# Performance work log

Measured on AMD Instinct MI355X. Metric: run time of the kernel, lower is better.

The kernel has to match this reference:

```python
import jax, jax.numpy as jnp
import numpy as np

HEADS = 20  # SDXL-style: hidden_size 1280 / head_dim 64
IP_SCALE = 1.0


def setup_inputs() -> dict:
    key = jax.random.key(0)
    ks = jax.random.split(key, 12)
    B, Sq, T, C, D, NIP = 4, 4096, 77, 1280, 2048, 16
    s = lambda fan: 1.0 / np.sqrt(fan)
    # post-softmax multiplicative mask: col 0 (sot token) forced to 1, rest a binary spatial mask
    spat = (jax.random.uniform(ks[0], (1, Sq, 1)) < 0.5).astype(jnp.float32)
    attention_mask = jnp.concatenate([jnp.ones((1, Sq, 1)), jnp.tile(spat, (1, 1, T - 1))], axis=-1)
    return {
        "hidden_states": jax.random.normal(ks[1], (B, Sq, C), jnp.float32),
        "encoder_hidden_states": jax.random.normal(ks[2], (B, T, D), jnp.float32),
        "ip_hidden_states": jax.random.normal(ks[3], (B, NIP, D), jnp.float32),
        "attention_mask": attention_mask,
        "Wq": jax.random.normal(ks[4], (C, C), jnp.float32) * s(C),
        "Wk": jax.random.normal(ks[5], (D, C), jnp.float32) * s(D),
        "Wv": jax.random.normal(ks[6], (D, C), jnp.float32) * s(D),
        "Wo": jax.random.normal(ks[7], (C, C), jnp.float32) * s(C),
        "bo": jnp.zeros((C,), jnp.float32),
        "Wk_ip": jax.random.normal(ks[8], (D, C), jnp.float32) * s(D),
        "Wv_ip": jax.random.normal(ks[9], (D, C), jnp.float32) * s(D),
    }


def reference(hidden_states, encoder_hidden_states, ip_hidden_states, attention_mask,
              Wq, Wk, Wv, Wo, bo, Wk_ip, Wv_ip):
    B, Sq, C = hidden_states.shape
    H = HEADS
    d = C // H
    scale = d ** -0.5
    # projections (torch Linear with weights stored [in, out])
    q = (hidden_states @ Wq).reshape(B, Sq, H, d)
    k = (encoder_hidden_states @ Wk).reshape(B, -1, H, d)
    v = (encoder_hidden_states @ Wv).reshape(B, -1, H, d)
    # explicit QK^T softmax, then POST-softmax multiplicative mask (as in get_attention_scores + mask multiply)
    scores = jnp.einsum('bqhd,bkhd->bhqk', q, k) * scale
    probs = jax.nn.softmax(scores, axis=-1)
    probs = probs * attention_mask[:, None, :, :]  # [1,1,Sq,T] broadcast over batch*heads
    out = jnp.einsum('bhqk,bkhd->bqhd', probs, v).reshape(B, Sq, C)
    out = out @ Wo + bo  # to_out[0]; to_out[1] is dropout (identity at eval)
    # IP-adapter stream (single stream, no spatial ip mask): standard SDPA against ip tokens
    k_ip = (ip_hidden_states @ Wk_ip).reshape(B, -1, H, d)
    v_ip = (ip_hidden_states @ Wv_ip).reshape(B, -1, H, d)
    s_ip = jnp.einsum('bqhd,bkhd->bhqk', q, k_ip) * scale
    p_ip = jax.nn.softmax(s_ip, axis=-1)
    ip_out = jnp.einsum('bhqk,bkhd->bqhd', p_ip, v_ip).reshape(B, Sq, C)
    return out + IP_SCALE * ip_out
```

## Files before the change

### kernel.cpp

```cpp
#include <hip/hip_runtime.h>

typedef __attribute__((ext_vector_type(4))) float f32x4;
typedef __attribute__((ext_vector_type(8))) short s16x8;
typedef __attribute__((ext_vector_type(8))) __bf16 bf16x8;
typedef unsigned short u16;

__device__ __forceinline__ u16 f2b(float f) {
  union { float f; unsigned u; } x; x.f = f;
  unsigned r = x.u + 0x7fffu + ((x.u >> 16) & 1u);
  return (u16)(r >> 16);
}
__device__ __forceinline__ float b2f(u16 u) {
  union { unsigned u; float f; } x; x.u = ((unsigned)u) << 16;
  return x.f;
}
__device__ __forceinline__ void gld16(const void* g, void* l) {
  __builtin_amdgcn_global_load_lds(
      (const __attribute__((address_space(1))) unsigned int*)g,
      (__attribute__((address_space(3))) unsigned int*)l, 16, 0, 0);
}
__device__ __forceinline__ f32x4 mfma_bf16(s16x8 a, s16x8 b, f32x4 c) {
  return __builtin_amdgcn_mfma_f32_16x16x32_bf16(
      __builtin_bit_cast(bf16x8, a), __builtin_bit_cast(bf16x8, b), c, 0, 0, 0);
}

#define BAR() asm volatile("s_barrier" ::: "memory")

__global__ void k_convert_all(const float* __restrict__ hs, const float* __restrict__ ehs,
                              const float* __restrict__ iph,
                              u16* __restrict__ hsb, u16* __restrict__ ehsb,
                              u16* __restrict__ ipb) {
  const int n1 = 16384 * 1280 / 4, n2 = 308 * 2048 / 4, n3 = 64 * 2048 / 4;
  int i = blockIdx.x * blockDim.x + threadIdx.x;
  const float* src; u16* dst; int j = i;
  if (i < n1) { src = hs; dst = hsb; }
  else if (i < n1 + n2) { src = ehs; dst = ehsb; j = i - n1; }
  else if (i < n1 + n2 + n3) { src = iph; dst = ipb; j = i - n1 - n2; }
  else return;
  float4 v = ((const float4*)src)[j];
  ushort4 o;
  o.x = f2b(v.x); o.y = f2b(v.y); o.z = f2b(v.z); o.w = f2b(v.w);
  ((ushort4*)dst)[j] = o;
}

__global__ void k_transpose_all(const float* Wk, const float* Wv, const float* Wkip,
                                const float* Wvip, const float* Wq, const float* Wo,
                                u16* TK, u16* TV, u16* TKip, u16* TVip,
                                u16* TQ, u16* TO) {
  const int z = blockIdx.z;
  const float* W = (z == 0) ? Wk : (z == 1) ? Wv : (z == 2) ? Wkip
                  : (z == 3) ? Wvip : (z == 4) ? Wq : Wo;
  u16* T = (z == 0) ? TK : (z == 1) ? TV : (z == 2) ? TKip
          : (z == 3) ? TVip : (z == 4) ? TQ : TO;
  const int K = (z < 4) ? 2048 : 1280;
  const int N = 1280;
  __shared__ float tile[32][33];
  int n0 = blockIdx.x * 32, k0 = blockIdx.y * 32;
  if (k0 >= K) return;
  int tx = threadIdx.x & 31, ty = threadIdx.x >> 5;
#pragma unroll
  for (int i = 0; i < 32; i += 8)
    tile[ty + i][tx] = W[(size_t)(k0 + ty + i) * N + n0 + tx];
  __syncthreads();
#pragma unroll
  for (int i = 0; i < 32; i += 8)
    T[(size_t)(n0 + ty + i) * K + k0 + tx] = f2b(tile[tx][ty + i]);
}

__device__ __forceinline__ void gemm_core0(
    const u16* __restrict__ A, const u16* __restrict__ BT,
    int M, int N, int K, u16* __restrict__ outb, int m0, int n0) {
  const int tid = threadIdx.x;
  const int l = tid & 63;
  const int w = tid >> 6;
  const int wr = w >> 1, wc = w & 1;
  __shared__ u16 As[3][128 * 32];
  __shared__ u16 Bs[3][128 * 32];
  f32x4 acc[4][4] = {};

  const int o0 = tid * 16;
  const int o1 = o0 + 4096;
  const int ra0 = o0 >> 6, ca0 = (o0 & 63) >> 1;
  const int ra1 = o1 >> 6, ca1 = (o1 & 63) >> 1;
  int ga0 = m0 + ra0; if (ga0 >= M) ga0 = M - 1;
  int ga1 = m0 + ra1; if (ga1 >= M) ga1 = M - 1;
  const u16* Ar0 = A + (size_t)ga0 * K + ca0;
  const u16* Ar1 = A + (size_t)ga1 * K + ca1;
  const u16* Br0 = BT + (size_t)(n0 + ra0) * K + ca0;
  const u16* Br1 = BT + (size_t)(n0 + ra1) * K + ca1;

  const int KT = K >> 5;
#define SSTAGE(s, kt)                                 \
  {                                                   \
    const int k0_ = (kt) << 5;                        \
    gld16(Ar0 + k0_, &As[s][o0 >> 1]);                \
    gld16(Ar1 + k0_, &As[s][o1 >> 1]);                \
    gld16(Br0 + k0_, &Bs[s][o0 >> 1]);                \
    gld16(Br1 + k0_, &Bs[s][o1 >> 1]);                \
  }
  SSTAGE(0, 0);
  SSTAGE(1, 1);
  asm volatile("s_waitcnt vmcnt(4)" ::: "memory");
  BAR();

  int slot = 0;
  for (int j = 0; j < KT; ++j) {
    const bool pf = (j + 2 < KT);
    if (pf) {
      int s2 = slot + 2; if (s2 >= 3) s2 -= 3;
      SSTAGE(s2, j + 2);
    }
    s16x8 af[4], bfr[4];
#pragma unroll
    for (int mi = 0; mi < 4; ++mi)
      af[mi] = *(const s16x8*)&As[slot][(wr * 64 + mi * 16 + (l & 15)) * 32 + (l >> 4) * 8];
#pragma unroll
    for (int ni = 0; ni < 4; ++ni)
      bfr[ni] = *(const s16x8*)&Bs[slot][(wc * 64 + ni * 16 + (l & 15)) * 32 + (l >> 4) * 8];
#pragma unroll
    for (int mi = 0; mi < 4; ++mi)
#pragma unroll
      for (int ni = 0; ni < 4; ++ni)
        acc[mi][ni] = mfma_bf16(af[mi], bfr[ni], acc[mi][ni]);
    if (pf) asm volatile("s_waitcnt vmcnt(4)" ::: "memory");
    else    asm volatile("s_waitcnt vmcnt(0)" ::: "memory");
    BAR();
    ++slot; if (slot >= 3) slot = 0;
  }

#pragma unroll
  for (int mi = 0; mi < 4; ++mi) {
    const int mbase = m0 + wr * 64 + mi * 16 + (l >> 4) * 4;
#pragma unroll
    for (int ni = 0; ni < 4; ++ni) {
      const int ncol = n0 + wc * 64 + ni * 16 + (l & 15);
#pragma unroll
      for (int r = 0; r < 4; ++r) {
        int m = mbase + r;
        if (m < M) outb[(size_t)m * N + ncol] = f2b(acc[mi][ni][r]);
      }
    }
  }
#undef SSTAGE
}

__global__ __launch_bounds__(256) void k_gemm_small4(
    const u16* __restrict__ ehsb, const u16* __restrict__ ipb,
    const u16* __restrict__ WkT, const u16* __restrict__ WvT,
    const u16* __restrict__ WkipT, const u16* __restrict__ WvipT,
    u16* kbuf, u16* vbuf, u16* kipb, u16* vipb) {
  const int z = blockIdx.z;
  const int M = (z < 2) ? 308 : 64;
  const int m0 = blockIdx.y * 128;
  if (m0 >= M) return;
  const u16* A = (z < 2) ? ehsb : ipb;
  const u16* BT = (z == 0) ? WkT : (z == 1) ? WvT : (z == 2) ? WkipT : WvipT;
  u16* out = (z == 0) ? kbuf : (z == 1) ? vbuf : (z == 2) ? kipb : vipb;
  gemm_core0(A, BT, M, 1280, 2048, out, m0, blockIdx.x * 128);
}

template <int EPI>
__global__ __launch_bounds__(512, 1) void k_gemm256(
    const u16* __restrict__ A, const u16* __restrict__ BT,
    int N, int K, float alpha,
    u16* __restrict__ outb, float* __restrict__ outf,
    const float* __restrict__ bias, const u16* __restrict__ ipadd,
    int nbx) {
  __shared__ u16 lds[73728];
  const int tid = threadIdx.x, l = tid & 63, w = tid >> 6;
  const int lr = l & 15, lg = l >> 4;
  const int wr = w >> 2, wc = w & 3;
  const bool wlo = (w < 4);

  const int nwg = gridDim.x;
  const int q = nwg >> 3, r = nwg & 7;
  const int xcd = blockIdx.x & 7, lid = blockIdx.x >> 3;
  const int wg = (xcd < r) ? (xcd * (q + 1) + lid)
                           : (r * (q + 1) + (xcd - r) * q + lid);
  const int bm0 = (wg / nbx) * 256, bn0 = (wg % nbx) * 320;

  const int srow = tid >> 2;
  const int sslot = ((tid & 3) ^ ((srow >> 1) & 3)) * 8;
  const size_t aO0 = (size_t)(bm0 + srow) * K + sslot;
  const size_t aO1 = aO0 + (size_t)128 * K;
  const size_t bO0 = (size_t)(bn0 + srow) * K + sslot;
  const size_t bO1 = bO0 + (size_t)128 * K;
  const size_t bO2 = bO0 + (size_t)256 * K;
  const int d0 = tid * 8, d1 = (tid + 512) * 8, d2 = (tid + 1024) * 8;

  const int KT = K >> 5;
  f32x4 acc[8][5] = {};
  s16x8 bfv[5], afv[4];

  const int xsw = (lg ^ ((lr >> 1) & 3)) * 8;
  const int aRow = (wr * 128 + lr) * 32 + xsw;
  const int bRow = 32768 + (wc * 80 + lr) * 32 + xsw;

#define STAGE_A(slot, kt)                                              \
  {                                                                    \
    const int base_ = (slot) * 8192;                                   \
    const size_t go_ = (size_t)(kt) * 32;                              \
    gld16(A + aO0 + go_, &lds[base_ + d0]);                            \
    gld16(A + aO1 + go_, &lds[base_ + d1]);                            \
  }
#define STAGE_B(slot, kt)                                              \
  {                                                                    \
    const int base_ = 32768 + (slot) * 10240;                          \
    const size_t go_ = (size_t)(kt) * 32;                              \
    gld16(BT + bO0 + go_, &lds[base_ + d0]);                           \
    gld16(BT + bO1 + go_, &lds[base_ + d1]);                           \
    if (wlo) gld16(BT + bO2 + go_, &lds[base_ + d2]);                  \
  }
#define WAIT_DEEP()                                                    \
  {                                                                    \
    if (wlo) asm volatile("s_waitcnt vmcnt(10)" ::: "memory");         \
    else     asm volatile("s_waitcnt vmcnt(8)" ::: "memory");          \
  }
#define WAIT_MID()                                                     \
  {                                                                    \
    if (wlo) asm volatile("s_waitcnt vmcnt(5)" ::: "memory");          \
    else     asm volatile("s_waitcnt vmcnt(4)" ::: "memory");          \
  }
#define WAITVM0() asm volatile("s_waitcnt vmcnt(0)" ::: "memory")

  STAGE_A(0, 0); STAGE_B(0, 0);
  STAGE_A(1, 1); STAGE_B(1, 1);
  STAGE_A(2, 2); STAGE_B(2, 2);
  WAIT_DEEP();
  BAR();

  for (int j = 0; j < KT; ++j) {
    const int slot = j & 3;
    const int ab = slot * 8192;
    const int bb = slot * 10240;
    const bool pf = (j + 3 < KT);
    const int s3 = (j + 3) & 3;
#pragma unroll
    for (int ni = 0; ni < 5; ++ni)
      bfv[ni] = *(const s16x8*)&lds[bb + bRow + ni * 512];
#pragma unroll
    for (int mi = 0; mi < 4; ++mi)
      afv[mi] = *(const s16x8*)&lds[ab + aRow + mi * 512];
    if (pf) STAGE_A(s3, j + 3);
    __builtin_amdgcn_s_setprio(1);
#pragma unroll
    for (int mi = 0; mi < 4; ++mi)
#pragma unroll
      for (int ni = 0; ni < 5; ++ni)
        acc[mi][ni] = mfma_bf16(afv[mi], bfv[ni], acc[mi][ni]);
    __builtin_amdgcn_s_setprio(0);
#pragma unroll
    for (int mi = 0; mi < 4; ++mi)
      afv[mi] = *(const s16x8*)&lds[ab + aRow + (mi + 4) * 512];
    if (pf) STAGE_B(s3, j + 3);
    __builtin_amdgcn_s_setprio(1);
#pragma unroll
    for (int mi = 0; mi < 4; ++mi)
#pragma unroll
      for (int ni = 0; ni < 5; ++ni)
        acc[mi + 4][ni] = mfma_bf16(afv[mi], bfv[ni], acc[mi + 4][ni]);
    __builtin_amdgcn_s_setprio(0);
    if (pf) { WAIT_DEEP(); }
    else if (j == KT - 3) { WAIT_MID(); }
    else { WAITVM0(); }
    BAR();
  }

  WAITVM0();
  __syncthreads();

  if constexpr (EPI == 0) {
#pragma unroll
    for (int half = 0; half < 2; ++half) {
      if (half) __syncthreads();
      if (wr == half) {
#pragma unroll
        for (int mi = 0; mi < 8; ++mi) {
          const int row = mi * 16 + lg * 4;
#pragma unroll
          for (int ni = 0; ni < 5; ++ni) {
            const int col = wc * 80 + ni * 16 + lr;
#pragma unroll
            for (int rr = 0; rr < 4; ++rr)
              lds[(row + rr) * 320 + col] = f2b(acc[mi][ni][rr] * alpha);
          }
        }
      }
      __syncthreads();
      const int rbase = tid >> 3;
      const int cseg = tid & 7;
#pragma unroll
      for (int rr2 = 0; rr2 < 2; ++rr2)
#pragma unroll
        for (int jj = 0; jj < 5; ++jj) {
          const int row = rr2 * 64 + rbase;
          const int ch = cseg + jj * 8;
          *(int4*)(outb + (size_t)(bm0 + half * 128 + row) * N + bn0 + ch * 8) =
              *(const int4*)&lds[row * 320 + ch * 8];
        }
    }
  } else {
#pragma unroll
    for (int mi = 0; mi < 8; ++mi) {
      const int mrow = bm0 + wr * 128 + mi * 16 + lg * 4;
#pragma unroll
      for (int ni = 0; ni < 5; ++ni) {
        const int ncol = bn0 + wc * 80 + ni * 16 + lr;
#pragma unroll
        for (int rr = 0; rr < 4; ++rr) {
          const size_t idx = (size_t)(mrow + rr) * N + ncol;
          outf[idx] = acc[mi][ni][rr] + bias[ncol] + b2f(ipadd[idx]);
        }
      }
    }
  }
#undef STAGE_A
#undef STAGE_B
#undef WAIT_DEEP
#undef WAIT_MID
#undef WAITVM0
}

__global__ __launch_bounds__(512, 4) void k_attn(
    const u16* __restrict__ Q,
    const u16* __restrict__ Kb,
    const u16* __restrict__ Vb,
    const u16* __restrict__ Kip,
    const u16* __restrict__ Vip,
    const float* __restrict__ mask,
    u16* __restrict__ Oattn,
    u16* __restrict__ Oip) {
  const int qt = blockIdx.x, h = blockIdx.y, b = blockIdx.z;
  const int tid = threadIdx.x, l = tid & 63, w = tid >> 6;
  const int lr = l & 15, lg = l >> 4;
  const int r0 = w * 16;
  const int m0 = b * 4096 + qt * 128;

  __shared__ u16 KV[192][72];
  __shared__ u16 Ps[128][104];
  __shared__ u16 P2s[128][40];

  const u16* qrow = Q + (size_t)(m0 + r0 + lr) * 1280 + h * 64;
  s16x8 aq0 = *(const s16x8*)(qrow + lg * 8);
  s16x8 aq1 = *(const s16x8*)(qrow + 32 + lg * 8);

  for (int s = tid; s < 192 * 8; s += 512) {
    const int row = s >> 3, seg = s & 7;
    int4 v = {0, 0, 0, 0};
    const u16* src = nullptr;
    if (row < 77)       src = Kb  + (size_t)(b * 77 + row) * 1280 + h * 64 + seg * 8;
    else if (row < 80)  src = nullptr;
    else if (row < 96)  src = Kip + (size_t)(b * 16 + row - 80) * 1280 + h * 64 + seg * 8;
    else if (row < 173) src = Vb  + (size_t)(b * 77 + row - 96) * 1280 + h * 64 + seg * 8;
    else if (row < 176) src = nullptr;
    else                src = Vip + (size_t)(b * 16 + row - 176) * 1280 + h * 64 + seg * 8;
    if (src) v = *(const int4*)src;
    *(int4*)&KV[row][(seg ^ ((row >> 3) & 3)) * 8] = v;
  }
  __syncthreads();

  f32x4 sc[5];
  f32x4 sip = {};
#pragma unroll
  for (int t5 = 0; t5 < 6; ++t5) {
    const int trow = t5 * 16 + lr;
    const int qz = (trow >> 3) & 3;
    s16x8 b0 = *(const s16x8*)&KV[trow][(lg ^ qz) * 8];
    s16x8 b1 = *(const s16x8*)&KV[trow][((lg + 4) ^ qz) * 8];
    f32x4 c = {};
    c = mfma_bf16(aq0, b0, c);
    c = mfma_bf16(aq1, b1, c);
    if (t5 < 5) sc[t5] = c; else sip = c;
  }

#pragma unroll
  for (int r = 0; r < 4; ++r) {
    float mx = fmaxf(fmaxf(fmaxf(sc[0][r], sc[1][r]), fmaxf(sc[2][r], sc[3][r])), sc[4][r]);
    mx = fmaxf(mx, __shfl_xor(mx, 1));
    mx = fmaxf(mx, __shfl_xor(mx, 2));
    mx = fmaxf(mx, __shfl_xor(mx, 4));
    mx = fmaxf(mx, __shfl_xor(mx, 8));
    float p[5], sm = 0.f;
#pragma unroll
    for (int t5 = 0; t5 < 5; ++t5) {
      bool valid = (t5 < 4) | (lr < 13);
      p[t5] = valid ? __expf(sc[t5][r] - mx) : 0.f;
      sm += p[t5];
    }
    sm += __shfl_xor(sm, 1);
    sm += __shfl_xor(sm, 2);
    sm += __shfl_xor(sm, 4);
    sm += __shfl_xor(sm, 8);
    const float inv = 1.0f / sm;
    const int row = r0 + lg * 4 + r;
    const int qg = qt * 128 + row;
#pragma unroll
    for (int t5 = 0; t5 < 5; ++t5) {
      int t = t5 * 16 + lr;
      float pf = 0.f;
      if (t < 77) pf = p[t5] * inv * mask[qg * 77 + t];
      Ps[row][t] = f2b(pf);
    }
    Ps[row][80 + lr] = 0;

    float m2 = sip[r];
    m2 = fmaxf(m2, __shfl_xor(m2, 1));
    m2 = fmaxf(m2, __shfl_xor(m2, 2));
    m2 = fmaxf(m2, __shfl_xor(m2, 4));
    m2 = fmaxf(m2, __shfl_xor(m2, 8));
    float pi = __expf(sip[r] - m2);
    float s2 = pi;
    s2 += __shfl_xor(s2, 1);
    s2 += __shfl_xor(s2, 2);
    s2 += __shfl_xor(s2, 4);
    s2 += __shfl_xor(s2, 8);
    P2s[row][lr] = 0;
    P2s[row][16 + lr] = f2b(pi / s2);
  }

  s16x8 ap[3];
#pragma unroll
  for (int ks = 0; ks < 3; ++ks)
    ap[ks] = *(const s16x8*)&Ps[r0 + lr][ks * 32 + lg * 8];
  s16x8 aip = *(const s16x8*)&P2s[r0 + lr][lg * 8];

  f32x4 om[4], oi[4];
#pragma unroll
  for (int nt = 0; nt < 4; ++nt) {
    const int dcol = (nt * 16 + lr) ^ (lg << 3);
    f32x4 o = {};
#pragma unroll
    for (int ks = 0; ks < 3; ++ks) {
      s16x8 bv;
#pragma unroll
      for (int j = 0; j < 8; ++j)
        bv[j] = (short)KV[96 + ks * 32 + lg * 8 + j][dcol];
      o = mfma_bf16(ap[ks], bv, o);
    }
    s16x8 bip;
#pragma unroll
    for (int j = 0; j < 8; ++j)
      bip[j] = (short)KV[160 + lg * 8 + j][dcol];
    f32x4 o2 = {};
    o2 = mfma_bf16(aip, bip, o2);
    om[nt] = o;
    oi[nt] = o2;
  }

  __syncthreads();

  u16 (*Om)[72] = (u16(*)[72]) & KV[0][0];
  u16 (*Oi)[72] = (u16(*)[72]) & Ps[0][0];
#pragma unroll
  for (int nt = 0; nt < 4; ++nt)
#pragma unroll
    for (int r = 0; r < 4; ++r) {
      const int row = r0 + lg * 4 + r;
      const int d = nt * 16 + lr;
      Om[row][d] = f2b(om[nt][r]);
      Oi[row][d] = f2b(oi[nt][r]);
    }
  __syncthreads();

  for (int s = tid; s < 128 * 8; s += 512) {
    const int row = s >> 3, seg = s & 7;
    const size_t g = (size_t)(m0 + row) * 1280 + h * 64 + seg * 8;
    *(int4*)(Oattn + g) = *(const int4*)&Om[row][seg * 8];
    *(int4*)(Oip + g) = *(const int4*)&Oi[row][seg * 8];
  }
}

extern "C" void kernel_launch(void* const* d_in, const int* in_sizes, int n_in,
                              void* d_out, int out_size, void* d_ws, size_t ws_size,
                              hipStream_t stream) {
  (void)in_sizes; (void)n_in; (void)out_size; (void)ws_size;
  const float* hs   = (const float*)d_in[0];
  const float* ehs  = (const float*)d_in[1];
  const float* iph  = (const float*)d_in[2];
  const float* mask = (const float*)d_in[3];
  const float* Wq   = (const float*)d_in[4];
  const float* Wk   = (const float*)d_in[5];
  const float* Wv   = (const float*)d_in[6];
  const float* Wo   = (const float*)d_in[7];
  const float* bo   = (const float*)d_in[8];
  const float* Wkip = (const float*)d_in[9];
  const float* Wvip = (const float*)d_in[10];
  float* out = (float*)d_out;

  char* ws = (char*)d_ws;
  size_t off = 0;
  auto alloc = [&](size_t bytes) {
    char* p = ws + off;
    off += (bytes + 255) & ~(size_t)255;
    return p;
  };
  u16* hsb   = (u16*)alloc(16384ull * 1280 * 2);
  u16* qbuf  = (u16*)alloc(16384ull * 1280 * 2);
  u16* ipout = (u16*)alloc(16384ull * 1280 * 2);
  u16* WqT   = (u16*)alloc(1280ull * 1280 * 2);
  u16* WoT   = (u16*)alloc(1280ull * 1280 * 2);
  u16* WkT   = (u16*)alloc(1280ull * 2048 * 2);
  u16* WvT   = (u16*)alloc(1280ull * 2048 * 2);
  u16* WkipT = (u16*)alloc(1280ull * 2048 * 2);
  u16* WvipT = (u16*)alloc(1280ull * 2048 * 2);
  u16* ehsb  = (u16*)alloc(308ull * 2048 * 2);
  u16* ipb   = (u16*)alloc(64ull * 2048 * 2);
  u16* kbuf  = (u16*)alloc(308ull * 1280 * 2);
  u16* vbuf  = (u16*)alloc(308ull * 1280 * 2);
  u16* kipb  = (u16*)alloc(64ull * 1280 * 2);
  u16* vipb  = (u16*)alloc(64ull * 1280 * 2);

  const int ntot4 = (16384 * 1280 + 308 * 2048 + 64 * 2048) / 4;
  k_convert_all<<<(ntot4 + 255) / 256, 256, 0, stream>>>(hs, ehs, iph, hsb, ehsb, ipb);
  k_transpose_all<<<dim3(40, 64, 6), 256, 0, stream>>>(Wk, Wv, Wkip, Wvip, Wq, Wo,
                                                       WkT, WvT, WkipT, WvipT, WqT, WoT);

  k_gemm256<0><<<256, 512, 0, stream>>>(hsb, WqT, 1280, 1280, 0.125f,
                                        qbuf, nullptr, nullptr, nullptr, 4);
  k_gemm_small4<<<dim3(10, 3, 4), 256, 0, stream>>>(ehsb, ipb, WkT, WvT, WkipT, WvipT,
                                                    kbuf, vbuf, kipb, vipb);

  k_attn<<<dim3(32, 20, 4), 512, 0, stream>>>(qbuf, kbuf, vbuf, kipb, vipb, mask,
                                              hsb, ipout);

  k_gemm256<1><<<256, 512, 0, stream>>>(hsb, WoT, 1280, 1280, 1.f,
                                        nullptr, out, bo, ipout, 4);
}
```

Baseline: 268.9 us.

## Pre-transpose V per head and deepen small-GEMM pipeline to five stages

Adds a kernel that writes V and V_ip transposed per head and batch into padded layouts. Attention can then read the PV MFMA B-operands with vector LDS loads instead of gathering eight scalar shorts per lane. Separately, the small K/V projection GEMM goes from a 3-slot to a 5-slot LDS ring with prefetch four tiles ahead and graded vmcnt waits. The cost is one extra kernel launch, extra global traffic for the transposed copies, and more LDS in the small GEMM.

Result: no change. 267.5 us (-0.5%).

```diff
diff --git a/kernel.cpp b/kernel.cpp
--- a/kernel.cpp
+++ b/kernel.cpp
@@ -74,8 +74,8 @@
   const int l = tid & 63;
   const int w = tid >> 6;
   const int wr = w >> 1, wc = w & 1;
-  __shared__ u16 As[3][128 * 32];
-  __shared__ u16 Bs[3][128 * 32];
+  __shared__ u16 As[5][4096];
+  __shared__ u16 Bs[5][4096];
   f32x4 acc[4][4] = {};
 
   const int o0 = tid * 16;
@@ -100,16 +100,14 @@
   }
   SSTAGE(0, 0);
   SSTAGE(1, 1);
-  asm volatile("s_waitcnt vmcnt(4)" ::: "memory");
+  SSTAGE(2, 2);
+  SSTAGE(3, 3);
+  asm volatile("s_waitcnt vmcnt(12)" ::: "memory");
   BAR();
 
-  int slot = 0;
+  int slot = 0, s4 = 4;
   for (int j = 0; j < KT; ++j) {
-    const bool pf = (j + 2 < KT);
-    if (pf) {
-      int s2 = slot + 2; if (s2 >= 3) s2 -= 3;
-      SSTAGE(s2, j + 2);
-    }
+    if (j + 4 < KT) SSTAGE(s4, j + 4);
     s16x8 af[4], bfr[4];
 #pragma unroll
     for (int mi = 0; mi < 4; ++mi)
@@ -122,10 +120,14 @@
 #pragma unroll
       for (int ni = 0; ni < 4; ++ni)
         acc[mi][ni] = mfma_bf16(af[mi], bfr[ni], acc[mi][ni]);
-    if (pf) asm volatile("s_waitcnt vmcnt(4)" ::: "memory");
-    else    asm volatile("s_waitcnt vmcnt(0)" ::: "memory");
+    const int rem = KT - 2 - j;
+    if (rem >= 3)      asm volatile("s_waitcnt vmcnt(12)" ::: "memory");
+    else if (rem == 2) asm volatile("s_waitcnt vmcnt(8)" ::: "memory");
+    else if (rem == 1) asm volatile("s_waitcnt vmcnt(4)" ::: "memory");
+    else               asm volatile("s_waitcnt vmcnt(0)" ::: "memory");
     BAR();
-    ++slot; if (slot >= 3) slot = 0;
+    ++slot; if (slot >= 5) slot = 0;
+    ++s4; if (s4 >= 5) s4 = 0;
   }
 
 #pragma unroll
@@ -159,6 +161,46 @@
   gemm_core0(A, BT, M, 1280, 2048, out, m0, blockIdx.x * 128);
 }
 
+__global__ void k_vtrans(const u16* __restrict__ vbuf, const u16* __restrict__ vipb,
+                         u16* __restrict__ vt, u16* __restrict__ vipt) {
+  const int b = blockIdx.x, h = blockIdx.y, z = blockIdx.z;
+  const int tid = threadIdx.x;
+  __shared__ u16 tile[80][72];
+  if (z == 0) {
+    for (int s = tid; s < 80 * 8; s += 256) {
+      int t = s >> 3, c = s & 7;
+      int4 v = {0, 0, 0, 0};
+      if (t < 77) v = *(const int4*)(vbuf + (size_t)(b * 77 + t) * 1280 + h * 64 + c * 8);
+      *(int4*)&tile[t][c * 8] = v;
+    }
+    __syncthreads();
+    for (int s = tid; s < 64 * 12; s += 256) {
+      int d = s / 12, tc = s % 12;
+      s16x8 v;
+#pragma unroll
+      for (int j = 0; j < 8; ++j) {
+        int t = tc * 8 + j;
+        v[j] = (t < 80) ? (short)tile[t][d] : (short)0;
+      }
+      *(s16x8*)(vt + ((size_t)(h * 64 + d) * 4 + b) * 96 + tc * 8) = v;
+    }
+  } else {
+    for (int s = tid; s < 16 * 8; s += 256) {
+      int t = s >> 3, c = s & 7;
+      *(int4*)&tile[t][c * 8] =
+          *(const int4*)(vipb + (size_t)(b * 16 + t) * 1280 + h * 64 + c * 8);
+    }
+    __syncthreads();
+    for (int s = tid; s < 64 * 2; s += 256) {
+      int d = s >> 1, tc = s & 1;
+      s16x8 v;
+#pragma unroll
+      for (int j = 0; j < 8; ++j) v[j] = (short)tile[tc * 8 + j][d];
+      *(s16x8*)(vipt + ((size_t)(h * 64 + d) * 4 + b) * 16 + tc * 8) = v;
+    }
+  }
+}
+
 template <int EPI>
 __global__ __launch_bounds__(512, 1) void k_gemm256(
     const u16* __restrict__ A, const u16* __restrict__ BT,
@@ -324,38 +366,47 @@
 __global__ __launch_bounds__(512, 4) void k_attn(
     const u16* __restrict__ Q,
     const u16* __restrict__ Kb,
-    const u16* __restrict__ Vb,
     const u16* __restrict__ Kip,
-    const u16* __restrict__ Vip,
+    const u16* __restrict__ Vt,
+    const u16* __restrict__ VipT,
     const float* __restrict__ mask,
-    u16* __restrict__ Oattn,
-    u16* __restrict__ Oip) {
+    u16* __restrict__ Oattn, u16* __restrict__ Oip) {
   const int qt = blockIdx.x, h = blockIdx.y, b = blockIdx.z;
   const int tid = threadIdx.x, l = tid & 63, w = tid >> 6;
   const int lr = l & 15, lg = l >> 4;
   const int r0 = w * 16;
   const int m0 = b * 4096 + qt * 128;
 
-  __shared__ u16 KV[192][72];
-  __shared__ u16 Ps[128][104];
-  __shared__ u16 P2s[128][40];
+  __shared__ u16 S[34560];
+  u16 (*Ks)[72] = (u16(*)[72]) & S[0];
+  const int VT_OFF = 6912, VIP_OFF = 13568;
+  u16 (*Ps)[104] = (u16(*)[104]) & S[16128];
+  u16 (*P2s)[40] = (u16(*)[40]) & S[29440];
 
   const u16* qrow = Q + (size_t)(m0 + r0 + lr) * 1280 + h * 64;
   s16x8 aq0 = *(const s16x8*)(qrow + lg * 8);
   s16x8 aq1 = *(const s16x8*)(qrow + 32 + lg * 8);
 
-  for (int s = tid; s < 192 * 8; s += 512) {
+  for (int s = tid; s < 96 * 8; s += 512) {
     const int row = s >> 3, seg = s & 7;
     int4 v = {0, 0, 0, 0};
-    const u16* src = nullptr;
-    if (row < 77)       src = Kb  + (size_t)(b * 77 + row) * 1280 + h * 64 + seg * 8;
-    else if (row < 80)  src = nullptr;
-    else if (row < 96)  src = Kip + (size_t)(b * 16 + row - 80) * 1280 + h * 64 + seg * 8;
-    else if (row < 173) src = Vb  + (size_t)(b * 77 + row - 96) * 1280 + h * 64 + seg * 8;
-    else if (row < 176) src = nullptr;
-    else                src = Vip + (size_t)(b * 16 + row - 176) * 1280 + h * 64 + seg * 8;
-    if (src) v = *(const int4*)src;
-    *(int4*)&KV[row][(seg ^ ((row >> 3) & 3)) * 8] = v;
+    if (row < 77)
+      v = *(const int4*)(Kb + (size_t)(b * 77 + row) * 1280 + h * 64 + seg * 8);
+    else if (row >= 80)
+      v = *(const int4*)(Kip + (size_t)(b * 16 + row - 80) * 1280 + h * 64 + seg * 8);
+    *(int4*)&Ks[row][(seg ^ ((row >> 3) & 3)) * 8] = v;
+  }
+  for (int s = tid; s < 64 * 12; s += 512) {
+    const int row = s / 12, c = s % 12;
+    *(int4*)&S[VT_OFF + row * 104 + c * 8] =
+        *(const int4*)(Vt + ((size_t)(h * 64 + row) * 4 + b) * 96 + c * 8);
+  }
+  for (int s = tid; s < 64 * 4; s += 512) {
+    const int row = s >> 2, c = s & 3;
+    int4 v = {0, 0, 0, 0};
+    if (c >= 2)
+      v = *(const int4*)(VipT + ((size_t)(h * 64 + row) * 4 + b) * 16 + (c - 2) * 8);
+    *(int4*)&S[VIP_OFF + row * 40 + c * 8] = v;
   }
   __syncthreads();
 
@@ -365,8 +416,8 @@
   for (int t5 = 0; t5 < 6; ++t5) {
     const int trow = t5 * 16 + lr;
     const int qz = (trow >> 3) & 3;
-    s16x8 b0 = *(const s16x8*)&KV[trow][(lg ^ qz) * 8];
-    s16x8 b1 = *(const s16x8*)&KV[trow][((lg + 4) ^ qz) * 8];
+    s16x8 b0 = *(const s16x8*)&Ks[trow][(lg ^ qz) * 8];
+    s16x8 b1 = *(const s16x8*)&Ks[trow][((lg + 4) ^ qz) * 8];
     f32x4 c = {};
     c = mfma_bf16(aq0, b0, c);
     c = mfma_bf16(aq1, b1, c);
@@ -427,20 +478,14 @@
   f32x4 om[4], oi[4];
 #pragma unroll
   for (int nt = 0; nt < 4; ++nt) {
-    const int dcol = (nt * 16 + lr) ^ (lg << 3);
+    const int vrow = nt * 16 + lr;
     f32x4 o = {};
 #pragma unroll
     for (int ks = 0; ks < 3; ++ks) {
-      s16x8 bv;
-#pragma unroll
-      for (int j = 0; j < 8; ++j)
-        bv[j] = (short)KV[96 + ks * 32 + lg * 8 + j][dcol];
+      s16x8 bv = *(const s16x8*)&S[VT_OFF + vrow * 104 + (ks * 4 + lg) * 8];
       o = mfma_bf16(ap[ks], bv, o);
     }
-    s16x8 bip;
-#pragma unroll
-    for (int j = 0; j < 8; ++j)
-      bip[j] = (short)KV[160 + lg * 8 + j][dcol];
+    s16x8 bip = *(const s16x8*)&S[VIP_OFF + vrow * 40 + lg * 8];
     f32x4 o2 = {};
     o2 = mfma_bf16(aip, bip, o2);
     om[nt] = o;
@@ -449,8 +494,8 @@
 
   __syncthreads();
 
-  u16 (*Om)[72] = (u16(*)[72]) & KV[0][0];
-  u16 (*Oi)[72] = (u16(*)[72]) & Ps[0][0];
+  u16 (*Om)[72] = (u16(*)[72]) & S[0];
+  u16 (*Oi)[72] = (u16(*)[72]) & S[16128];
 #pragma unroll
   for (int nt = 0; nt < 4; ++nt)
 #pragma unroll
@@ -509,6 +554,8 @@
   u16* vbuf  = (u16*)alloc(308ull * 1280 * 2);
   u16* kipb  = (u16*)alloc(64ull * 1280 * 2);
   u16* vipb  = (u16*)alloc(64ull * 1280 * 2);
+  u16* vt    = (u16*)alloc(1280ull * 4 * 96 * 2);
+  u16* vipt  = (u16*)alloc(1280ull * 4 * 16 * 2);
 
   const int ntot4 = (16384 * 1280 + 308 * 2048 + 64 * 2048) / 4;
   k_convert_all<<<(ntot4 + 255) / 256, 256, 0, stream>>>(hs, ehs, iph, hsb, ehsb, ipb);
@@ -519,8 +566,9 @@
                                         qbuf, nullptr, nullptr, nullptr, 4);
   k_gemm_small4<<<dim3(10, 3, 4), 256, 0, stream>>>(ehsb, ipb, WkT, WvT, WkipT, WvipT,
                                                     kbuf, vbuf, kipb, vipb);
-
-  k_attn<<<dim3(32, 20, 4), 512, 0, stream>>>(qbuf, kbuf, vbuf, kipb, vipb, mask,
+  k_vtrans<<<dim3(4, 20, 2), 256, 0, stream>>>(vbuf, vipb, vt, vipt);
+
+  k_attn<<<dim3(32, 20, 4), 512, 0, stream>>>(qbuf, kbuf, kipb, vt, vipt, mask,
                                               hsb, ipout);
 
   k_gemm256<1><<<256, 512, 0, stream>>>(hsb, WoT, 1280, 1280, 1.f,
```
